# Performance work log

Hardware: AMD Instinct MI355X
Metric: run time of the kernel (lower is better)

## Reference

```python
import jax, jax.numpy as jnp
import numpy as np

EPS = 0.5
GAM1 = 1.0
GAM2 = 1.0
GAM3 = 1.0


def setup_inputs() -> dict:
    key = jax.random.key(0)
    k1, k2, k3 = jax.random.split(key, 3)
    n, d, C = 8192, 512, 10
    Z = jax.random.normal(k1, (n, d), dtype=jnp.float32)
    Z_bar = jax.random.normal(k2, (n, d), dtype=jnp.float32)
    real_label = jax.random.randint(k3, (n,), 0, C)
    return {"Z": Z, "Z_bar": Z_bar, "real_label": real_label, "num_classes": C}


def _mcr_terms(Z, Z_bar, real_label, num_classes):
    n, d = Z.shape
    dtype = Z.dtype
    Pi = jax.nn.one_hot(real_label, num_classes, dtype=dtype)  # [n, C]
    counts = Pi.sum(axis=0)                                    # [C]
    I = jnp.eye(d, dtype=dtype)

    # Discriminative terms: logdet(I + d/(n*eps) * Z^T Z) / 2
    disc_z = jnp.linalg.slogdet(I + (d / (n * EPS)) * (Z.T @ Z))[1] / 2.0
    disc_zb = jnp.linalg.slogdet(I + (d / (n * EPS)) * (Z_bar.T @ Z_bar))[1] / 2.0

    # Per-class Grams: Z[:, mask_j] @ Z[:, mask_j].T == Z^T diag(Pi[:,j]) Z
    Gz = jnp.einsum('nc,nd,ne->cde', Pi, Z, Z)          # [C, d, d]
    Gzb = jnp.einsum('nc,nd,ne->cde', Pi, Z_bar, Z_bar)  # [C, d, d]

    trPi = counts + 1e-8                                 # matches torch's +1e-08
    scal = (d / (trPi * EPS))[:, None, None]
    ld_z = jnp.linalg.slogdet(I[None] + scal * Gz)[1]    # raw logdets (not halved)
    ld_zb = jnp.linalg.slogdet(I[None] + scal * Gzb)[1]
    s = trPi / (2.0 * n)
    comp_z = jnp.sum(s * ld_z)
    comp_zb = jnp.sum(s * ld_zb)

    z_total = -(disc_z - comp_z)
    zb_total = -(disc_zb - comp_zb)

    # R(z_j, zbar_j): concat rows -> Gram sum, n_j = 2*count_j (exact count)
    n_j = 2.0 * counts
    scal3 = (d / (n_j * EPS))[:, None, None]
    ld3 = jnp.linalg.slogdet(I[None] + scal3 * (Gz + Gzb))[1] / 2.0
    item = jnp.sum(ld3)

    term3 = item - 0.25 * jnp.sum(ld_z) - 0.25 * jnp.sum(ld_zb)
    errD = -(GAM1 * (disc_z - comp_z) + GAM2 * (disc_zb - comp_zb) + GAM3 * term3)
    return errD, z_total, zb_total, term3


def reference(Z, Z_bar, real_label, num_classes):
    errD, z_total, zb_total, term3 = _mcr_terms(Z, Z_bar, real_label, num_classes)
    # empi = [z_total, zbar_total, term3]; pack everything into one vector
    return jnp.stack([errD, z_total, zb_total, term3])
```

## Files before the change

### kernel.cpp

```cpp
#include <hip/hip_runtime.h>
#include <math.h>

#define NROWS 8192
#define DIM   512
#define NCLS  10
#define GT    4
#define GPAIR 10
#define NMAT  32

typedef __attribute__((ext_vector_type(8))) short bf16x8;
typedef __attribute__((ext_vector_type(4))) float f32x4;

__device__ __forceinline__ float rdlane(float v, int l) {
    return __int_as_float(__builtin_amdgcn_readlane(__float_as_int(v), l));
}

__global__ __launch_bounds__(256) void k_count(const int* __restrict__ label,
                                               int* __restrict__ counts,
                                               int* __restrict__ lists) {
    __shared__ int hist[NCLS];
    __shared__ int base[NCLS];
    __shared__ int lofs[NCLS];
    int tid = threadIdx.x;
    int i = blockIdx.x * 256 + tid;
    if (tid < NCLS) { hist[tid] = 0; lofs[tid] = 0; }
    __syncthreads();
    int c = label[i];
    atomicAdd(&hist[c], 1);
    __syncthreads();
    if (tid < NCLS) base[tid] = atomicAdd(&counts[tid], hist[tid]);
    __syncthreads();
    int lpos = atomicAdd(&lofs[c], 1);
    lists[(size_t)c * NROWS + base[c] + lpos] = i;
}

__global__ __launch_bounds__(512) void k_gram(const float* __restrict__ Z,
                                              const float* __restrict__ Zb,
                                              const int* __restrict__ counts,
                                              const int* __restrict__ lists,
                                              float* __restrict__ G) {
    int pt = blockIdx.x;
    int c  = blockIdx.y;
    int tz = blockIdx.z;
    int ti = 0, tj = 0;
    { int p = pt;
      for (int r = 0; r < GT; ++r) { if (p <= r) { ti = r; tj = p; break; } p -= (r + 1); } }
    bool diag = (ti == tj);

    const float* __restrict__ src = tz ? Zb : Z;
    float* __restrict__ Gout = G + (((size_t)tz * NCLS + c) * GPAIR + pt) * 16384;
    int cnt = counts[c];
    const int* __restrict__ list = lists + (size_t)c * NROWS;

    __shared__ float As[2][16][132];
    __shared__ float Bs[2][16][132];
    int tid = threadIdx.x;
    int gid = tid >> 8;
    int t   = tid & 255;
    int tx = t & 15, ty = t >> 4;
    int srow = t >> 4, sc4 = t & 15;

    float acc[8][8];
    #pragma unroll
    for (int r = 0; r < 8; ++r)
        #pragma unroll
        for (int s = 0; s < 8; ++s) acc[r][s] = 0.f;

    for (int base0 = 0; base0 < cnt; base0 += 32) {
        int gr = base0 + gid * 16 + srow;
        float4 va0 = make_float4(0.f, 0.f, 0.f, 0.f), va1 = va0, vb0 = va0, vb1 = va0;
        if (gr < cnt) {
            int ridx = list[gr];
            const float* __restrict__ rp = src + (size_t)ridx * DIM;
            va0 = *(const float4*)&rp[ti * 128 + sc4 * 4];
            va1 = *(const float4*)&rp[ti * 128 + 64 + sc4 * 4];
            if (!diag) {
                vb0 = *(const float4*)&rp[tj * 128 + sc4 * 4];
                vb1 = *(const float4*)&rp[tj * 128 + 64 + sc4 * 4];
            }
        }
        *(float4*)&As[gid][srow][sc4 * 4]      = va0;
        *(float4*)&As[gid][srow][64 + sc4 * 4] = va1;
        if (!diag) {
            *(float4*)&Bs[gid][srow][sc4 * 4]      = vb0;
            *(float4*)&Bs[gid][srow][64 + sc4 * 4] = vb1;
        }
        __syncthreads();

        const float (*__restrict__ Ap)[132] = As[gid];
        const float (*__restrict__ Bp)[132] = diag ? As[gid] : Bs[gid];
        #pragma unroll
        for (int kk = 0; kk < 16; ++kk) {
            float a[8], b[8];
            *(float4*)&a[0] = *(const float4*)&Ap[kk][ty * 4];
            *(float4*)&a[4] = *(const float4*)&Ap[kk][64 + ty * 4];
            *(float4*)&b[0] = *(const float4*)&Bp[kk][tx * 4];
            *(float4*)&b[4] = *(const float4*)&Bp[kk][64 + tx * 4];
            #pragma unroll
            for (int r = 0; r < 8; ++r)
                #pragma unroll
                for (int s = 0; s < 8; ++s)
                    acc[r][s] += a[r] * b[s];
        }
        __syncthreads();
    }

    float* red = (float*)&As[0][0][0];
    #pragma unroll
    for (int r = 0; r < 8; ++r) {
        __syncthreads();
        if (gid == 1) {
            #pragma unroll
            for (int s = 0; s < 8; ++s) red[t * 8 + s] = acc[r][s];
        }
        __syncthreads();
        if (gid == 0) {
            #pragma unroll
            for (int s = 0; s < 8; ++s) acc[r][s] += red[t * 8 + s];
        }
    }
    if (gid == 0) {
        #pragma unroll
        for (int r = 0; r < 8; ++r) {
            int row = (r < 4) ? (ty * 4 + r) : (64 + ty * 4 + r - 4);
            float4 v0 = make_float4(acc[r][0], acc[r][1], acc[r][2], acc[r][3]);
            float4 v1 = make_float4(acc[r][4], acc[r][5], acc[r][6], acc[r][7]);
            *(float4*)&Gout[(size_t)row * 128 + tx * 4]      = v0;
            *(float4*)&Gout[(size_t)row * 128 + 64 + tx * 4] = v1;
        }
    }
}

__global__ __launch_bounds__(256) void k_assemble(const float* __restrict__ G,
                                                  const int* __restrict__ counts,
                                                  float* __restrict__ A) {
    int pt = blockIdx.x;
    int m  = blockIdx.y;
    int ti = 0, tj = 0;
    { int p = pt;
      for (int r = 0; r < GT; ++r) { if (p <= r) { ti = r; tj = p; break; } p -= (r + 1); } }

    const size_t TILE = 16384;
    const float* __restrict__ Gz  = G;
    const float* __restrict__ Gzb = G + (size_t)NCLS * GPAIR * TILE;
    float* __restrict__ Am = A + (size_t)m * DIM * DIM;
    int tid = threadIdx.x;

    int mode; int c; float sc;
    if (m < 10)      { mode = 0; c = m;      sc = 1024.f / ((float)counts[c] + 1e-8f); }
    else if (m < 20) { mode = 1; c = m - 10; sc = 1024.f / ((float)counts[c] + 1e-8f); }
    else if (m < 30) { mode = 2; c = m - 20; sc = 512.f / (float)counts[c]; }
    else             { mode = (m == 30) ? 3 : 4; c = 0; sc = 0.125f; }

    #pragma unroll 1
    for (int h = 0; h < 16; ++h) {
        int id = h * 256 + tid;
        int row = id >> 5, c4 = id & 31;
        size_t off = (size_t)row * 128 + c4 * 4;
        float4 g = make_float4(0.f, 0.f, 0.f, 0.f);
        if (mode == 0) {
            g = *(const float4*)&Gz[((size_t)c * GPAIR + pt) * TILE + off];
        } else if (mode == 1) {
            g = *(const float4*)&Gzb[((size_t)c * GPAIR + pt) * TILE + off];
        } else if (mode == 2) {
            float4 a = *(const float4*)&Gz [((size_t)c * GPAIR + pt) * TILE + off];
            float4 b = *(const float4*)&Gzb[((size_t)c * GPAIR + pt) * TILE + off];
            g.x = a.x + b.x; g.y = a.y + b.y; g.z = a.z + b.z; g.w = a.w + b.w;
        } else if (mode == 3) {
            for (int cc = 0; cc < NCLS; ++cc) {
                float4 t = *(const float4*)&Gz[((size_t)cc * GPAIR + pt) * TILE + off];
                g.x += t.x; g.y += t.y; g.z += t.z; g.w += t.w;
            }
        } else {
            for (int cc = 0; cc < NCLS; ++cc) {
                float4 t = *(const float4*)&Gzb[((size_t)cc * GPAIR + pt) * TILE + off];
                g.x += t.x; g.y += t.y; g.z += t.z; g.w += t.w;
            }
        }
        g.x *= sc; g.y *= sc; g.z *= sc; g.w *= sc;
        if (ti == tj) {
            int cb = c4 * 4;
            if (row == cb)     g.x += 1.f;
            if (row == cb + 1) g.y += 1.f;
            if (row == cb + 2) g.z += 1.f;
            if (row == cb + 3) g.w += 1.f;
        }
        *(float4*)&Am[(size_t)(ti * 128 + row) * DIM + tj * 128 + c4 * 4] = g;
    }
}

__global__ __launch_bounds__(512) void k_chol(float* __restrict__ A,
                                              float* __restrict__ ld) {
    int m = blockIdx.x;
    float* __restrict__ Am = A + (size_t)m * DIM * DIM;
    int tid = threadIdx.x;
    int wave = tid >> 6, lane = tid & 63;

    __shared__ float  Dl[64][68];
    __shared__ float  dinv[64];
    __shared__ ushort Thi[448][64];
    __shared__ ushort Tlo[448][64];

    #pragma unroll 1
    for (int p = 0; p < 8; ++p) {
        int col0 = p * 64, col1 = col0 + 64;
        int mt = DIM - col1;
        int K = mt >> 6;
        int chunk = wave - 1;
        bool is_trsm = (chunk >= 0 && chunk < K);

        for (int h = tid; h < 1024; h += 512) {
            int r = h >> 4, c4 = h & 15;
            *(float4*)&Dl[r][c4 * 4] = *(const float4*)&Am[(size_t)(col0 + r) * DIM + col0 + c4 * 4];
        }
        __syncthreads();

        if (wave == 0) {
            float row_[64];
            #pragma unroll
            for (int j = 0; j < 64; ++j) row_[j] = Dl[lane][j];
            float dval = 1.f;
            #pragma unroll
            for (int k = 0; k < 64; ++k) {
                float piv = rdlane(row_[k], k);
                float s = 1.0f / sqrtf(piv);
                float lik = row_[k] * s;
                dval = (lane == k) ? lik : dval;
                row_[k] = lik;
                #pragma unroll
                for (int j = k + 1; j < 64; ++j)
                    row_[j] -= lik * rdlane(lik, j);
            }
            #pragma unroll
            for (int j = 0; j < 64; ++j) Dl[lane][j] = row_[j];
            dinv[lane] = 1.f / dval;
            float v = 2.f * logf(dval);
            #pragma unroll
            for (int off = 32; off > 0; off >>= 1) v += __shfl_down(v, off);
            if (lane == 0) atomicAdd(&ld[m], v);
        }
        __syncthreads();

        if (is_trsm) {
            float Lreg[64];
            #pragma unroll
            for (int j4 = 0; j4 < 16; ++j4)
                *(float4*)&Lreg[j4 * 4] = *(const float4*)&Dl[lane][j4 * 4];
            float dv = dinv[lane];
            const float* __restrict__ Brow = Am + (size_t)(col1 + chunk * 64 + lane) * DIM + col0;
            float t[64];
            float4 bv;
            #pragma unroll
            for (int i = 0; i < 64; ++i) {
                if ((i & 3) == 0) bv = *(const float4*)&Brow[i];
                float a0 = (i & 3) == 0 ? bv.x : ((i & 3) == 1 ? bv.y : ((i & 3) == 2 ? bv.z : bv.w));
                float a1 = 0.f, a2 = 0.f, a3 = 0.f;
                int mm = 0;
                #pragma unroll
                for (; mm + 3 < i; mm += 4) {
                    a0 -= t[mm]     * rdlane(Lreg[mm],     i);
                    a1 -= t[mm + 1] * rdlane(Lreg[mm + 1], i);
                    a2 -= t[mm + 2] * rdlane(Lreg[mm + 2], i);
                    a3 -= t[mm + 3] * rdlane(Lreg[mm + 3], i);
                }
                #pragma unroll
                for (; mm < i; ++mm) a0 -= t[mm] * rdlane(Lreg[mm], i);
                t[i] = ((a0 + a1) + (a2 + a3)) * rdlane(dv, i);
            }
            int row = chunk * 64 + lane;
            int hsw = (row & 7) << 3;
            #pragma unroll
            for (int i = 0; i < 64; i += 2) {
                uint u0 = __float_as_uint(t[i]);
                float h0f = __uint_as_float(u0 & 0xFFFF0000u);
                uint l0 = __float_as_uint(t[i] - h0f);
                uint u1 = __float_as_uint(t[i + 1]);
                float h1f = __uint_as_float(u1 & 0xFFFF0000u);
                uint l1 = __float_as_uint(t[i + 1] - h1f);
                int idx = i ^ hsw;
                *(uint*)&Thi[row][idx] = (u0 >> 16) | (u1 & 0xFFFF0000u);
                *(uint*)&Tlo[row][idx] = (l0 >> 16) | (l1 & 0xFFFF0000u);
            }
        }
        __syncthreads();

        if (K > 0) {
            int lr = lane & 15, kb = lane >> 4;
            int npair = K * (K + 1) / 2;
            for (int tix = wave; tix < npair; tix += 8) {
                int a = 0, b = 0;
                { int q = tix;
                  for (int r0 = 0; r0 < 7; ++r0) { if (q <= r0) { a = r0; b = q; break; } q -= (r0 + 1); } }
                f32x4 acc[4][4];
                #pragma unroll
                for (int it = 0; it < 4; ++it)
                    #pragma unroll
                    for (int jt = 0; jt < 4; ++jt)
                        acc[it][jt] = (f32x4){0.f, 0.f, 0.f, 0.f};
                #pragma unroll
                for (int k0 = 0; k0 < 64; k0 += 32) {
                    bf16x8 Ah[4], Al[4], Bh[4], Bl[4];
                    int idx = (k0 + kb * 8) ^ ((lr & 7) << 3);
                    #pragma unroll
                    for (int it = 0; it < 4; ++it) {
                        int rowA = a * 64 + it * 16 + lr;
                        Ah[it] = *(const bf16x8*)&Thi[rowA][idx];
                        Al[it] = *(const bf16x8*)&Tlo[rowA][idx];
                        int rowB = b * 64 + it * 16 + lr;
                        Bh[it] = *(const bf16x8*)&Thi[rowB][idx];
                        Bl[it] = *(const bf16x8*)&Tlo[rowB][idx];
                    }
                    #pragma unroll
                    for (int it = 0; it < 4; ++it)
                        #pragma unroll
                        for (int jt = 0; jt < 4; ++jt) {
                            acc[it][jt] = __builtin_amdgcn_mfma_f32_16x16x32_bf16(Ah[it], Bh[jt], acc[it][jt], 0, 0, 0);
                            acc[it][jt] = __builtin_amdgcn_mfma_f32_16x16x32_bf16(Ah[it], Bl[jt], acc[it][jt], 0, 0, 0);
                            acc[it][jt] = __builtin_amdgcn_mfma_f32_16x16x32_bf16(Al[it], Bh[jt], acc[it][jt], 0, 0, 0);
                        }
                }
                #pragma unroll
                for (int it = 0; it < 4; ++it)
                    #pragma unroll
                    for (int jt = 0; jt < 4; ++jt)
                        #pragma unroll
                        for (int rg = 0; rg < 4; ++rg) {
                            int gi = col1 + a * 64 + it * 16 + kb * 4 + rg;
                            int gj = col1 + b * 64 + jt * 16 + lr;
                            Am[(size_t)gi * DIM + gj] -= acc[it][jt][rg];
                        }
            }
        }
        __syncthreads();
    }
}

__global__ void k_final(const float* __restrict__ ld,
                        const int* __restrict__ counts,
                        float* __restrict__ out) {
    if (threadIdx.x == 0 && blockIdx.x == 0) {
        float disc_z  = 0.5f * ld[30];
        float disc_zb = 0.5f * ld[31];
        float comp_z = 0.f, comp_zb = 0.f, sum_ldz = 0.f, sum_ldzb = 0.f, item = 0.f;
        for (int c = 0; c < NCLS; ++c) {
            float trPi = (float)counts[c] + 1e-8f;
            float s = trPi / (2.f * (float)NROWS);
            comp_z  += s * ld[c];
            comp_zb += s * ld[10 + c];
            sum_ldz  += ld[c];
            sum_ldzb += ld[10 + c];
            item += 0.5f * ld[20 + c];
        }
        float term3 = item - 0.25f * sum_ldz - 0.25f * sum_ldzb;
        float z_total  = -(disc_z - comp_z);
        float zb_total = -(disc_zb - comp_zb);
        float errD = -((disc_z - comp_z) + (disc_zb - comp_zb) + term3);
        out[0] = errD; out[1] = z_total; out[2] = zb_total; out[3] = term3;
    }
}

extern "C" void kernel_launch(void* const* d_in, const int* in_sizes, int n_in,
                              void* d_out, int out_size, void* d_ws, size_t ws_size,
                              hipStream_t stream) {
    (void)in_sizes; (void)n_in; (void)out_size; (void)ws_size;
    const float* Z     = (const float*)d_in[0];
    const float* Zb    = (const float*)d_in[1];
    const int*   label = (const int*)d_in[2];

    char* ws = (char*)d_ws;
    int*   counts = (int*)ws;
    float* ld     = (float*)(ws + 64);
    int*   lists  = (int*)(ws + 256);
    float* G      = (float*)(ws + 256 + (size_t)NCLS * NROWS * 4);
    float* A      = G + (size_t)2 * NCLS * GPAIR * 16384;
    float* out    = (float*)d_out;

    hipMemsetAsync(ws, 0, 256, stream);
    k_count<<<NROWS / 256, 256, 0, stream>>>(label, counts, lists);
    k_gram<<<dim3(GPAIR, NCLS, 2), 512, 0, stream>>>(Z, Zb, counts, lists, G);
    k_assemble<<<dim3(GPAIR, NMAT), 256, 0, stream>>>(G, counts, A);
    k_chol<<<NMAT, 512, 0, stream>>>(A, ld);
    k_final<<<1, 64, 0, stream>>>(ld, counts, out);
}
```

Baseline: 571.8 us.

## Prefetch gram tiles with doubled K-chunk and look-ahead next-panel Cholesky factorization

The Gram kernel now stages 32 rows per group, 64 per block iteration, and prefetches the next chunk's global loads into registers while the current chunk is computed. This is meant to hide global-memory latency and halve the number of barriers. The Cholesky kernel adds a look-ahead step: wave 0 computes the next diagonal block's update itself with MFMA and factors it immediately, while the other 7 waves update the remaining trailing tiles. This takes the serial panel factorization off the critical path, at the cost of more LDS in the Gram kernel and one fewer wave for the trailing update.

```diff
diff --git a/kernel.cpp b/kernel.cpp
--- a/kernel.cpp
+++ b/kernel.cpp
@@ -13,6 +13,31 @@
 
 __device__ __forceinline__ float rdlane(float v, int l) {
     return __int_as_float(__builtin_amdgcn_readlane(__float_as_int(v), l));
+}
+
+__device__ __forceinline__ void fact64(float (*Dl)[68], float* dinv, float* ldm, int lane) {
+    float row_[64];
+    #pragma unroll
+    for (int j = 0; j < 64; ++j) row_[j] = Dl[lane][j];
+    float dval = 1.f;
+    #pragma unroll
+    for (int k = 0; k < 64; ++k) {
+        float piv = rdlane(row_[k], k);
+        float s = 1.0f / sqrtf(piv);
+        float lik = row_[k] * s;
+        dval = (lane == k) ? lik : dval;
+        row_[k] = lik;
+        #pragma unroll
+        for (int j = k + 1; j < 64; ++j)
+            row_[j] -= lik * rdlane(lik, j);
+    }
+    #pragma unroll
+    for (int j = 0; j < 64; ++j) Dl[lane][j] = row_[j];
+    dinv[lane] = 1.f / dval;
+    float v = 2.f * logf(dval);
+    #pragma unroll
+    for (int off = 32; off > 0; off >>= 1) v += __shfl_down(v, off);
+    if (lane == 0) atomicAdd(ldm, v);
 }
 
 __global__ __launch_bounds__(256) void k_count(const int* __restrict__ label,
@@ -52,13 +77,13 @@
     int cnt = counts[c];
     const int* __restrict__ list = lists + (size_t)c * NROWS;
 
-    __shared__ float As[2][16][132];
-    __shared__ float Bs[2][16][132];
+    __shared__ float As[2][32][132];
+    __shared__ float Bs[2][32][132];
     int tid = threadIdx.x;
     int gid = tid >> 8;
     int t   = tid & 255;
     int tx = t & 15, ty = t >> 4;
-    int srow = t >> 4, sc4 = t & 15;
+    int sr = t >> 3, se = t & 7;
 
     float acc[8][8];
     #pragma unroll
@@ -66,31 +91,45 @@
         #pragma unroll
         for (int s = 0; s < 8; ++s) acc[r][s] = 0.f;
 
-    for (int base0 = 0; base0 < cnt; base0 += 32) {
-        int gr = base0 + gid * 16 + srow;
-        float4 va0 = make_float4(0.f, 0.f, 0.f, 0.f), va1 = va0, vb0 = va0, vb1 = va0;
+    float4 pa[4], pb[4];
+    {
+        int gr = gid * 32 + sr;
+        #pragma unroll
+        for (int q = 0; q < 4; ++q) { pa[q] = make_float4(0.f,0.f,0.f,0.f); pb[q] = pa[q]; }
         if (gr < cnt) {
-            int ridx = list[gr];
-            const float* __restrict__ rp = src + (size_t)ridx * DIM;
-            va0 = *(const float4*)&rp[ti * 128 + sc4 * 4];
-            va1 = *(const float4*)&rp[ti * 128 + 64 + sc4 * 4];
-            if (!diag) {
-                vb0 = *(const float4*)&rp[tj * 128 + sc4 * 4];
-                vb1 = *(const float4*)&rp[tj * 128 + 64 + sc4 * 4];
-            }
-        }
-        *(float4*)&As[gid][srow][sc4 * 4]      = va0;
-        *(float4*)&As[gid][srow][64 + sc4 * 4] = va1;
-        if (!diag) {
-            *(float4*)&Bs[gid][srow][sc4 * 4]      = vb0;
-            *(float4*)&Bs[gid][srow][64 + sc4 * 4] = vb1;
-        }
-        __syncthreads();
-
+            const float* __restrict__ rp = src + (size_t)list[gr] * DIM;
+            #pragma unroll
+            for (int q = 0; q < 4; ++q) {
+                pa[q] = *(const float4*)&rp[ti * 128 + se * 16 + q * 4];
+                if (!diag) pb[q] = *(const float4*)&rp[tj * 128 + se * 16 + q * 4];
+            }
+        }
+    }
+
+    for (int base0 = 0; base0 < cnt; base0 += 64) {
+        #pragma unroll
+        for (int q = 0; q < 4; ++q) {
+            *(float4*)&As[gid][sr][se * 16 + q * 4] = pa[q];
+            if (!diag) *(float4*)&Bs[gid][sr][se * 16 + q * 4] = pb[q];
+        }
+        __syncthreads();
+        {
+            int gr = base0 + 64 + gid * 32 + sr;
+            #pragma unroll
+            for (int q = 0; q < 4; ++q) { pa[q] = make_float4(0.f,0.f,0.f,0.f); pb[q] = pa[q]; }
+            if (gr < cnt) {
+                const float* __restrict__ rp = src + (size_t)list[gr] * DIM;
+                #pragma unroll
+                for (int q = 0; q < 4; ++q) {
+                    pa[q] = *(const float4*)&rp[ti * 128 + se * 16 + q * 4];
+                    if (!diag) pb[q] = *(const float4*)&rp[tj * 128 + se * 16 + q * 4];
+                }
+            }
+        }
         const float (*__restrict__ Ap)[132] = As[gid];
         const float (*__restrict__ Bp)[132] = diag ? As[gid] : Bs[gid];
         #pragma unroll
-        for (int kk = 0; kk < 16; ++kk) {
+        for (int kk = 0; kk < 32; ++kk) {
             float a[8], b[8];
             *(float4*)&a[0] = *(const float4*)&Ap[kk][ty * 4];
             *(float4*)&a[4] = *(const float4*)&Ap[kk][64 + ty * 4];
@@ -189,8 +228,8 @@
     }
 }
 
-__global__ __launch_bounds__(512) void k_chol(float* __restrict__ A,
-                                              float* __restrict__ ld) {
+__global__ __launch_bounds__(512, 2) void k_chol(float* __restrict__ A,
+                                                 float* __restrict__ ld) {
     int m = blockIdx.x;
     float* __restrict__ Am = A + (size_t)m * DIM * DIM;
     int tid = threadIdx.x;
@@ -201,47 +240,23 @@
     __shared__ ushort Thi[448][64];
     __shared__ ushort Tlo[448][64];
 
+    for (int h = tid; h < 1024; h += 512) {
+        int r = h >> 4, c4 = h & 15;
+        *(float4*)&Dl[r][c4 * 4] = *(const float4*)&Am[(size_t)r * DIM + c4 * 4];
+    }
+    __syncthreads();
+    if (wave == 0) fact64(Dl, dinv, &ld[m], lane);
+    __syncthreads();
+
     #pragma unroll 1
-    for (int p = 0; p < 8; ++p) {
+    for (int p = 0; p < 7; ++p) {
         int col0 = p * 64, col1 = col0 + 64;
         int mt = DIM - col1;
         int K = mt >> 6;
+        int npair = K * (K + 1) / 2;
+
         int chunk = wave - 1;
-        bool is_trsm = (chunk >= 0 && chunk < K);
-
-        for (int h = tid; h < 1024; h += 512) {
-            int r = h >> 4, c4 = h & 15;
-            *(float4*)&Dl[r][c4 * 4] = *(const float4*)&Am[(size_t)(col0 + r) * DIM + col0 + c4 * 4];
-        }
-        __syncthreads();
-
-        if (wave == 0) {
-            float row_[64];
-            #pragma unroll
-            for (int j = 0; j < 64; ++j) row_[j] = Dl[lane][j];
-            float dval = 1.f;
-            #pragma unroll
-            for (int k = 0; k < 64; ++k) {
-                float piv = rdlane(row_[k], k);
-                float s = 1.0f / sqrtf(piv);
-                float lik = row_[k] * s;
-                dval = (lane == k) ? lik : dval;
-                row_[k] = lik;
-                #pragma unroll
-                for (int j = k + 1; j < 64; ++j)
-                    row_[j] -= lik * rdlane(lik, j);
-            }
-            #pragma unroll
-            for (int j = 0; j < 64; ++j) Dl[lane][j] = row_[j];
-            dinv[lane] = 1.f / dval;
-            float v = 2.f * logf(dval);
-            #pragma unroll
-            for (int off = 32; off > 0; off >>= 1) v += __shfl_down(v, off);
-            if (lane == 0) atomicAdd(&ld[m], v);
-        }
-        __syncthreads();
-
-        if (is_trsm) {
+        if (chunk >= 0 && chunk < K) {
             float Lreg[64];
             #pragma unroll
             for (int j4 = 0; j4 < 16; ++j4)
@@ -284,10 +299,47 @@
         }
         __syncthreads();
 
-        if (K > 0) {
-            int lr = lane & 15, kb = lane >> 4;
-            int npair = K * (K + 1) / 2;
-            for (int tix = wave; tix < npair; tix += 8) {
+        int lr = lane & 15, kb = lane >> 4;
+        if (wave == 0) {
+            f32x4 acc[4][4];
+            #pragma unroll
+            for (int it = 0; it < 4; ++it)
+                #pragma unroll
+                for (int jt = 0; jt < 4; ++jt)
+                    acc[it][jt] = (f32x4){0.f, 0.f, 0.f, 0.f};
+            #pragma unroll
+            for (int k0 = 0; k0 < 64; k0 += 32) {
+                bf16x8 Ah[4], Al[4];
+                int idx = (k0 + kb * 8) ^ ((lr & 7) << 3);
+                #pragma unroll
+                for (int it = 0; it < 4; ++it) {
+                    int rowA = it * 16 + lr;
+                    Ah[it] = *(const bf16x8*)&Thi[rowA][idx];
+                    Al[it] = *(const bf16x8*)&Tlo[rowA][idx];
+                }
+                #pragma unroll
+                for (int it = 0; it < 4; ++it)
+                    #pragma unroll
+                    for (int jt = 0; jt < 4; ++jt) {
+                        acc[it][jt] = __builtin_amdgcn_mfma_f32_16x16x32_bf16(Ah[it], Ah[jt], acc[it][jt], 0, 0, 0);
+                        acc[it][jt] = __builtin_amdgcn_mfma_f32_16x16x32_bf16(Ah[it], Al[jt], acc[it][jt], 0, 0, 0);
+                        acc[it][jt] = __builtin_amdgcn_mfma_f32_16x16x32_bf16(Al[it], Ah[jt], acc[it][jt], 0, 0, 0);
+                    }
+            }
+            #pragma unroll
+            for (int it = 0; it < 4; ++it)
+                #pragma unroll
+                for (int jt = 0; jt < 4; ++jt)
+                    #pragma unroll
+                    for (int rg = 0; rg < 4; ++rg) {
+                        int r = it * 16 + kb * 4 + rg;
+                        int cg = jt * 16 + lr;
+                        float orig = Am[(size_t)(col1 + r) * DIM + col1 + cg];
+                        Dl[r][cg] = orig - acc[it][jt][rg];
+                    }
+            fact64(Dl, dinv, &ld[m], lane);
+        } else {
+            for (int tix = wave; tix < npair; tix += 7) {
                 int a = 0, b = 0;
                 { int q = tix;
                   for (int r0 = 0; r0 < 7; ++r0) { if (q <= r0) { a = r0; b = q; break; } q -= (r0 + 1); } }
```

After: 509.0 us. 11.0% less time.
